# Performance work log

Hardware: AMD Instinct MI355X
Metric: run time of the kernel (lower is better)

## Reference

```python
import jax, jax.numpy as jnp
import numpy as np

NUM_SWEEPS = 200
BETA_MIN = 0.1
BETA_MAX = 5.0


def _anneal(thetas, Jsym, key):
    """Batched simulated annealing over Ising spins in {-1,+1}.

    thetas: [B, N] per-sample biases h; Jsym: [N, N] symmetric couplings.
    Vectorized Metropolis: each sweep, every spin is a flip candidate with
    prob 1/2 (random mask decorrelates simultaneous flips) and is accepted
    with prob min(1, exp(-beta * dE)).
    """
    B, N = thetas.shape
    k0, kloop = jax.random.split(key)
    s0 = jnp.where(jax.random.bernoulli(k0, 0.5, (B, N)), 1.0, -1.0).astype(thetas.dtype)
    betas = jnp.geomspace(BETA_MIN, BETA_MAX, NUM_SWEEPS).astype(thetas.dtype)

    def sweep(carry, beta):
        s, k = carry
        k, k1, k2 = jax.random.split(k, 3)
        # local field: h_i + sum_j Jsym_ij s_j  -> dE for flipping spin i
        local = thetas + s @ Jsym  # [B, N]
        dE = -2.0 * s * local
        accept = jax.random.uniform(k1, (B, N), dtype=s.dtype) < jnp.exp(-beta * dE)
        mask = jax.random.bernoulli(k2, 0.5, (B, N))
        s = jnp.where(accept & mask, -s, s)
        return (s, k), None

    (s, _), _ = jax.lax.scan(sweep, (s0, kloop), betas)
    return s


def setup_inputs() -> dict:
    key = jax.random.key(0)
    k1, k2 = jax.random.split(key)
    B, N = 4096, 256
    thetas = jax.random.normal(k1, (B, N), dtype=jnp.float32)
    gamma = jax.random.normal(k2, (N, N), dtype=jnp.float32) * 0.1
    return {"thetas": thetas, "gamma": gamma}


def reference(thetas, gamma):
    # couplings: strictly upper triangle of gamma (i < j), as in gamma_to_couplings
    J = jnp.triu(gamma, 1)
    Jsym = J + J.T
    s = _anneal(thetas, Jsym, jax.random.key(42))  # [B, N] spins in {-1,+1}
    # Ising energy: E = sum_i h_i s_i + sum_{i<j} J_ij s_i s_j
    energies = jnp.sum(s * thetas, axis=1) + 0.5 * jnp.einsum("bi,ij,bj->b", s, Jsym, s)
    return energies
```

## Files before the change

kernel.cpp:

```cpp
#include <hip/hip_runtime.h>
#include <stdint.h>
#include <math.h>

#define PARTITIONABLE 1

namespace {

constexpr int kB = 4096;
constexpr int kN = 256;
constexpr int kSweeps = 200;
constexpr int kSamp = 16;
constexpr int kBlocks = kB / kSamp;

struct K2 { uint32_t a, b; };

__host__ __device__ constexpr uint32_t crotl(uint32_t x, int d) {
  return (x << d) | (x >> (32 - d));
}

__host__ __device__ constexpr K2 ctf(uint32_t k0, uint32_t k1, uint32_t c0, uint32_t c1) {
  uint32_t ks0 = k0, ks1 = k1, ks2 = k0 ^ k1 ^ 0x1BD11BDAu;
  uint32_t x0 = c0 + ks0, x1 = c1 + ks1;
  const int r0[4] = {13, 15, 26, 6};
  const int r1[4] = {17, 29, 16, 24};
  for (int i = 0; i < 4; ++i) { x0 += x1; x1 = crotl(x1, r0[i]); x1 ^= x0; }
  x0 += ks1; x1 += ks2 + 1u;
  for (int i = 0; i < 4; ++i) { x0 += x1; x1 = crotl(x1, r1[i]); x1 ^= x0; }
  x0 += ks2; x1 += ks0 + 2u;
  for (int i = 0; i < 4; ++i) { x0 += x1; x1 = crotl(x1, r0[i]); x1 ^= x0; }
  x0 += ks0; x1 += ks1 + 3u;
  for (int i = 0; i < 4; ++i) { x0 += x1; x1 = crotl(x1, r1[i]); x1 ^= x0; }
  x0 += ks1; x1 += ks2 + 4u;
  for (int i = 0; i < 4; ++i) { x0 += x1; x1 = crotl(x1, r0[i]); x1 ^= x0; }
  x0 += ks2; x1 += ks0 + 5u;
  return K2{x0, x1};
}

struct KeyTable {
  uint32_t s0k[2];
  uint32_t sk[kSweeps][4];
};

constexpr KeyTable make_keys() {
  KeyTable t{};
  K2 root{0u, 42u};
#if PARTITIONABLE
  K2 k0 = ctf(root.a, root.b, 0u, 0u);
  K2 kl = ctf(root.a, root.b, 0u, 1u);
#else
  K2 p0 = ctf(root.a, root.b, 0u, 2u);
  K2 p1 = ctf(root.a, root.b, 1u, 3u);
  K2 k0{p0.a, p1.a};
  K2 kl{p0.b, p1.b};
#endif
  t.s0k[0] = k0.a; t.s0k[1] = k0.b;
  K2 k = kl;
  for (int s = 0; s < kSweeps; ++s) {
#if PARTITIONABLE
    K2 kn = ctf(k.a, k.b, 0u, 0u);
    K2 k1 = ctf(k.a, k.b, 0u, 1u);
    K2 k2 = ctf(k.a, k.b, 0u, 2u);
#else
    K2 q0 = ctf(k.a, k.b, 0u, 3u);
    K2 q1 = ctf(k.a, k.b, 1u, 4u);
    K2 q2 = ctf(k.a, k.b, 2u, 5u);
    K2 kn{q0.a, q1.a};
    K2 k1{q2.a, q0.b};
    K2 k2{q1.b, q2.b};
#endif
    t.sk[s][0] = k1.a; t.sk[s][1] = k1.b;
    t.sk[s][2] = k2.a; t.sk[s][3] = k2.b;
    k = kn;
  }
  return t;
}

__constant__ KeyTable g_keys = make_keys();

__device__ __forceinline__ uint32_t rng_bits32(uint32_t ka, uint32_t kb, uint32_t m) {
#if PARTITIONABLE
  K2 r = ctf(ka, kb, 0u, m);
  return r.a ^ r.b;
#else
  constexpr uint32_t H = (uint32_t)(kB * kN / 2);
  uint32_t p = (m < H) ? m : (m - H);
  K2 r = ctf(ka, kb, p, p + H);
  return (m < H) ? r.a : r.b;
#endif
}

__device__ __forceinline__ float bits_to_uniform(uint32_t bits) {
  return __uint_as_float((bits >> 9) | 0x3f800000u) - 1.0f;
}

__global__ void prep_kernel(const float* __restrict__ gamma,
                            float* __restrict__ jp,
                            float* __restrict__ betas) {
  int e = blockIdx.x * blockDim.x + threadIdx.x;
  int i = e / kN, j = e % kN;
  float v = 0.0f;
  if (i < j) v = gamma[i * kN + j];
  else if (i > j) v = gamma[j * kN + i];
  int rh = i >> 7, l = (i & 127) >> 1, r = i & 1, c = j >> 3, f = j & 7;
  jp[((rh * 32 + c) * 64 + l) * 16 + r * 8 + f] = v;
  if (e < kSweeps) {
    double l0 = log(0.1), l1 = log(5.0);
    betas[e] = (float)exp(l0 + (l1 - l0) * (double)e / (double)(kSweeps - 1));
  }
}

#define FMIX_LO(a, w, j)                                                      \
  asm("v_fma_mix_f32 %0, %1, %2, %0 op_sel:[0,0,0] op_sel_hi:[1,0,0]"         \
      : "+v"(a) : "v"(w), "v"(j))
#define FMIX_HI(a, w, j)                                                      \
  asm("v_fma_mix_f32 %0, %1, %2, %0 op_sel:[1,0,0] op_sel_hi:[1,0,0]"         \
      : "+v"(a) : "v"(w), "v"(j))

__global__ __launch_bounds__(512) void anneal_kernel(
    const float* __restrict__ thetas, const float* __restrict__ jp,
    const float* __restrict__ betas, float* __restrict__ out) {
  __shared__ __align__(16) unsigned short sh_h[2][kSamp][kN];
  __shared__ __align__(16) uint32_t sh_rand[2][kSamp * kN];
  __shared__ float sh_red[kSamp][4];

  const int tid = threadIdx.x;
  const int lane = tid & 63;
  const int wvid = tid >> 6;
  const bool consumer = (wvid < 4);
  const int b0 = blockIdx.x * kSamp;

  int cur = 0;

  if (consumer) {
    const int cw = wvid;
    const int oct = cw & 1;
    const int rh = cw >> 1;
    const int gbase = oct * 8;
    const int row0 = rh * 128 + 2 * lane;

    float th_[16];
    uint32_t sreg[8];
#pragma unroll
    for (int g = 0; g < 8; ++g) {
      float2 t2 = *(const float2*)&thetas[(b0 + gbase + g) * kN + row0];
      th_[2 * g] = t2.x; th_[2 * g + 1] = t2.y;
    }
#pragma unroll
    for (int g = 0; g < 8; ++g) {
      uint32_t m0 = (uint32_t)((b0 + gbase + g) * kN + row0);
      float u0 = bits_to_uniform(rng_bits32(g_keys.s0k[0], g_keys.s0k[1], m0));
      float u1 = bits_to_uniform(rng_bits32(g_keys.s0k[0], g_keys.s0k[1], m0 + 1));
      uint32_t pk = ((u0 < 0.5f) ? 0x3C00u : 0xBC00u) |
                    (((u1 < 0.5f) ? 0x3C00u : 0xBC00u) << 16);
      sreg[g] = pk;
      *(uint32_t*)&sh_h[0][gbase + g][row0] = pk;
    }
    __syncthreads();

    const float4* __restrict__ jpt =
        (const float4*)jp + (size_t)rh * 8192 + (size_t)lane * 4;

#define LDSPIN(g, c) (*(const uint4*)&sh_h[cur][gbase + (g)][(c) * 8])
#define CONSUME2(W, Q0, Q1, Q2, Q3)                                           \
  _Pragma("unroll")                                                           \
  for (int g = 0; g < 8; ++g) {                                               \
    FMIX_LO(acc[2*g], W[g].x, Q0.x); FMIX_HI(acc[2*g], W[g].x, Q0.y);         \
    FMIX_LO(acc[2*g], W[g].y, Q0.z); FMIX_HI(acc[2*g], W[g].y, Q0.w);         \
    FMIX_LO(acc[2*g], W[g].z, Q1.x); FMIX_HI(acc[2*g], W[g].z, Q1.y);         \
    FMIX_LO(acc[2*g], W[g].w, Q1.z); FMIX_HI(acc[2*g], W[g].w, Q1.w);         \
    FMIX_LO(acc[2*g+1], W[g].x, Q2.x); FMIX_HI(acc[2*g+1], W[g].x, Q2.y);     \
    FMIX_LO(acc[2*g+1], W[g].y, Q2.z); FMIX_HI(acc[2*g+1], W[g].y, Q2.w);     \
    FMIX_LO(acc[2*g+1], W[g].z, Q3.x); FMIX_HI(acc[2*g+1], W[g].z, Q3.y);     \
    FMIX_LO(acc[2*g+1], W[g].w, Q3.z); FMIX_HI(acc[2*g+1], W[g].w, Q3.w);     \
  }
#define MATVEC(acc)                                                           \
  {                                                                           \
    uint4 A[8], Bw[8];                                                        \
    float4 a0, a1, a2, a3, b0_, b1_, b2_, b3_;                                \
    _Pragma("unroll")                                                         \
    for (int g = 0; g < 8; ++g) A[g] = LDSPIN(g, 0);                          \
    a0 = jpt[0]; a1 = jpt[1]; a2 = jpt[2]; a3 = jpt[3];                       \
    _Pragma("unroll 1")                                                       \
    for (int k = 0; k < 15; ++k) {                                            \
      const int c = 2 * k;                                                    \
      _Pragma("unroll")                                                       \
      for (int g = 0; g < 8; ++g) Bw[g] = LDSPIN(g, c + 1);                   \
      b0_ = jpt[(c + 1) * 256 + 0]; b1_ = jpt[(c + 1) * 256 + 1];             \
      b2_ = jpt[(c + 1) * 256 + 2]; b3_ = jpt[(c + 1) * 256 + 3];             \
      CONSUME2(A, a0, a1, a2, a3)                                             \
      _Pragma("unroll")                                                       \
      for (int g = 0; g < 8; ++g) A[g] = LDSPIN(g, c + 2);                    \
      a0 = jpt[(c + 2) * 256 + 0]; a1 = jpt[(c + 2) * 256 + 1];               \
      a2 = jpt[(c + 2) * 256 + 2]; a3 = jpt[(c + 2) * 256 + 3];               \
      CONSUME2(Bw, b0_, b1_, b2_, b3_)                                        \
    }                                                                         \
    _Pragma("unroll")                                                         \
    for (int g = 0; g < 8; ++g) Bw[g] = LDSPIN(g, 31);                        \
    b0_ = jpt[31 * 256 + 0]; b1_ = jpt[31 * 256 + 1];                         \
    b2_ = jpt[31 * 256 + 2]; b3_ = jpt[31 * 256 + 3];                         \
    CONSUME2(A, a0, a1, a2, a3)                                               \
    CONSUME2(Bw, b0_, b1_, b2_, b3_)                                          \
  }

#pragma unroll 1
    for (int t = 0; t < kSweeps; ++t) {
      const float beta = betas[t];
      uint2 wp[8];
      {
        const uint32_t* __restrict__ rb =
            &sh_rand[t & 1][gbase * kN + rh * 128 + 2 * lane];
#pragma unroll
        for (int g = 0; g < 8; ++g)
          wp[g] = *(const uint2*)&rb[g * kN];
      }

      float acc[16];
#pragma unroll
      for (int x = 0; x < 16; ++x) acc[x] = 0.0f;
      MATVEC(acc)

#pragma unroll
      for (int g = 0; g < 8; ++g) {
        uint32_t pk = sreg[g];
        float s0f = __uint_as_float(0x3F800000u | ((pk << 16) & 0x80000000u));
        float s1f = __uint_as_float(0x3F800000u | (pk & 0x80000000u));
        float l0 = th_[2 * g] + acc[2 * g];
        float l1 = th_[2 * g + 1] + acc[2 * g + 1];
        float d0 = -2.0f * s0f * l0;
        float d1 = -2.0f * s1f * l1;
        float p0 = expf(-beta * d0);
        float p1 = expf(-beta * d1);
        float u0 = __uint_as_float((wp[g].x >> 1) | 0x3f800000u) - 1.0f;
        float u1 = __uint_as_float((wp[g].y >> 1) | 0x3f800000u) - 1.0f;
        uint32_t msk = 0u;
        if ((u0 < p0) && ((wp[g].x & 1u) == 0u)) msk |= 0x8000u;
        if ((u1 < p1) && ((wp[g].y & 1u) == 0u)) msk |= 0x80000000u;
        pk ^= msk;
        sreg[g] = pk;
        *(uint32_t*)&sh_h[cur ^ 1][gbase + g][row0] = pk;
      }
      __syncthreads();
      cur ^= 1;
    }

    {
      float acc[16];
#pragma unroll
      for (int x = 0; x < 16; ++x) acc[x] = 0.0f;
      MATVEC(acc)

#pragma unroll
      for (int g = 0; g < 8; ++g) {
        uint32_t pk = sreg[g];
        float s0f = __uint_as_float(0x3F800000u | ((pk << 16) & 0x80000000u));
        float s1f = __uint_as_float(0x3F800000u | (pk & 0x80000000u));
        float x0 = s0f * th_[2 * g] + 0.5f * (s0f * acc[2 * g]);
        float x1 = s1f * th_[2 * g + 1] + 0.5f * (s1f * acc[2 * g + 1]);
#pragma unroll
        for (int off = 16; off > 0; off >>= 1) {
          x0 += __shfl_down(x0, off);
          x1 += __shfl_down(x1, off);
        }
        float v = x0 + x1;
        if (lane == 0)  sh_red[gbase + g][2 * rh + 0] = v;
        if (lane == 32) sh_red[gbase + g][2 * rh + 1] = v;
      }
    }
  } else {
    const int p = (wvid - 4) * 64 + lane;
    {
      const uint32_t k1a = g_keys.sk[0][0], k1b = g_keys.sk[0][1];
      const uint32_t k2a = g_keys.sk[0][2], k2b = g_keys.sk[0][3];
      const uint32_t mb = (uint32_t)(b0 * kN + p * 16);
#pragma unroll 4
      for (int q = 0; q < 16; ++q) {
        uint32_t b1 = rng_bits32(k1a, k1b, mb + q);
        uint32_t b2 = rng_bits32(k2a, k2b, mb + q);
        sh_rand[0][p * 16 + q] = ((b1 >> 9) << 1) | (b2 >> 31);
      }
    }
    __syncthreads();

#pragma unroll 1
    for (int t = 0; t < kSweeps; ++t) {
      if (t + 1 < kSweeps) {
        const uint32_t k1a = g_keys.sk[t + 1][0], k1b = g_keys.sk[t + 1][1];
        const uint32_t k2a = g_keys.sk[t + 1][2], k2b = g_keys.sk[t + 1][3];
        const uint32_t mb = (uint32_t)(b0 * kN + p * 16);
        uint32_t wv[16];
#pragma unroll 4
        for (int q = 0; q < 16; ++q) {
          uint32_t b1 = rng_bits32(k1a, k1b, mb + q);
          uint32_t b2 = rng_bits32(k2a, k2b, mb + q);
          wv[q] = ((b1 >> 9) << 1) | (b2 >> 31);
        }
        uint32_t* dst = &sh_rand[(t + 1) & 1][p * 16];
#pragma unroll
        for (int q = 0; q < 4; ++q) {
          uint4 v; v.x = wv[4*q]; v.y = wv[4*q+1]; v.z = wv[4*q+2]; v.w = wv[4*q+3];
          *(uint4*)(dst + 4 * q) = v;
        }
      }
      __syncthreads();
    }
  }

  __syncthreads();
  if (tid < kSamp) {
    out[b0 + tid] =
        sh_red[tid][0] + sh_red[tid][1] + sh_red[tid][2] + sh_red[tid][3];
  }
}

}

extern "C" void kernel_launch(void* const* d_in, const int* in_sizes, int n_in,
                              void* d_out, int out_size, void* d_ws, size_t ws_size,
                              hipStream_t stream) {
  const float* thetas = (const float*)d_in[0];
  const float* gamma  = (const float*)d_in[1];
  float* jp    = (float*)d_ws;
  float* betas = (float*)((char*)d_ws + kN * kN * sizeof(float));

  hipLaunchKernelGGL(prep_kernel, dim3(kN), dim3(kN), 0, stream, gamma, jp, betas);
  hipLaunchKernelGGL(anneal_kernel, dim3(kBlocks), dim3(512), 0, stream,
                     thetas, jp, betas, (float*)d_out);
}
```

Baseline: 2.218 ms.

## Retile sweep matvec so each wave covers 4 samples across all 256 spins

```diff
diff --git a/kernel.cpp b/kernel.cpp
--- a/kernel.cpp
+++ b/kernel.cpp
@@ -94,18 +94,22 @@
 }
 
 __global__ void prep_kernel(const float* __restrict__ gamma,
-                            float* __restrict__ jp,
+                            float* __restrict__ jpA,
+                            float* __restrict__ jpB,
                             float* __restrict__ betas) {
   int e = blockIdx.x * blockDim.x + threadIdx.x;
   int i = e / kN, j = e % kN;
   float v = 0.0f;
   if (i < j) v = gamma[i * kN + j];
   else if (i > j) v = gamma[j * kN + i];
-  int rh = i >> 7, l = (i & 127) >> 1, r = i & 1, c = j >> 3, f = j & 7;
-  jp[((rh * 32 + c) * 64 + l) * 16 + r * 8 + f] = v;
+  int c = j >> 3, f = j & 7;
+  int l = i >> 2, rp = (i >> 1) & 1, rr = i & 1;
+  jpA[(((c * 64 + l) * 2 + rp) * 2 + rr) * 8 + f] = v;
+  int rh = i >> 7, l2 = (i & 127) >> 1, r = i & 1;
+  jpB[((rh * 32 + c) * 64 + l2) * 16 + r * 8 + f] = v;
   if (e < kSweeps) {
-    double l0 = log(0.1), l1 = log(5.0);
-    betas[e] = (float)exp(l0 + (l1 - l0) * (double)e / (double)(kSweeps - 1));
+    double lo = log(0.1), hi = log(5.0);
+    betas[e] = (float)exp(lo + (hi - lo) * (double)e / (double)(kSweeps - 1));
   }
 }
 
@@ -117,8 +121,9 @@
       : "+v"(a) : "v"(w), "v"(j))
 
 __global__ __launch_bounds__(512) void anneal_kernel(
-    const float* __restrict__ thetas, const float* __restrict__ jp,
-    const float* __restrict__ betas, float* __restrict__ out) {
+    const float* __restrict__ thetas, const float* __restrict__ jpA,
+    const float* __restrict__ jpB, const float* __restrict__ betas,
+    float* __restrict__ out) {
   __shared__ __align__(16) unsigned short sh_h[2][kSamp][kN];
   __shared__ __align__(16) uint32_t sh_rand[2][kSamp * kN];
   __shared__ float sh_red[kSamp][4];
@@ -133,137 +138,191 @@
 
   if (consumer) {
     const int cw = wvid;
-    const int oct = cw & 1;
-    const int rh = cw >> 1;
-    const int gbase = oct * 8;
-    const int row0 = rh * 128 + 2 * lane;
-
-    float th_[16];
-    uint32_t sreg[8];
-#pragma unroll
-    for (int g = 0; g < 8; ++g) {
-      float2 t2 = *(const float2*)&thetas[(b0 + gbase + g) * kN + row0];
-      th_[2 * g] = t2.x; th_[2 * g + 1] = t2.y;
-    }
-#pragma unroll
-    for (int g = 0; g < 8; ++g) {
+    const int gbase = cw * 4;
+    const int row0 = 4 * lane;
+
+    float4 th4[4];
+    uint2 sreg[4];
+#pragma unroll
+    for (int g = 0; g < 4; ++g)
+      th4[g] = *(const float4*)&thetas[(b0 + gbase + g) * kN + row0];
+
+#pragma unroll
+    for (int g = 0; g < 4; ++g) {
       uint32_t m0 = (uint32_t)((b0 + gbase + g) * kN + row0);
-      float u0 = bits_to_uniform(rng_bits32(g_keys.s0k[0], g_keys.s0k[1], m0));
-      float u1 = bits_to_uniform(rng_bits32(g_keys.s0k[0], g_keys.s0k[1], m0 + 1));
-      uint32_t pk = ((u0 < 0.5f) ? 0x3C00u : 0xBC00u) |
-                    (((u1 < 0.5f) ? 0x3C00u : 0xBC00u) << 16);
-      sreg[g] = pk;
-      *(uint32_t*)&sh_h[0][gbase + g][row0] = pk;
+      uint32_t h[4];
+#pragma unroll
+      for (int r = 0; r < 4; ++r) {
+        float u = bits_to_uniform(
+            rng_bits32(g_keys.s0k[0], g_keys.s0k[1], m0 + r));
+        h[r] = (u < 0.5f) ? 0x3C00u : 0xBC00u;
+      }
+      sreg[g].x = h[0] | (h[1] << 16);
+      sreg[g].y = h[2] | (h[3] << 16);
+      *(uint2*)&sh_h[0][gbase + g][row0] = sreg[g];
     }
     __syncthreads();
 
-    const float4* __restrict__ jpt =
-        (const float4*)jp + (size_t)rh * 8192 + (size_t)lane * 4;
-
-#define LDSPIN(g, c) (*(const uint4*)&sh_h[cur][gbase + (g)][(c) * 8])
-#define CONSUME2(W, Q0, Q1, Q2, Q3)                                           \
+    const float4* __restrict__ jpt = (const float4*)jpA + (size_t)lane * 8;
+
+#define LDSPIN4(g, c) (*(const uint4*)&sh_h[cur][gbase + (g)][(c) * 8])
+#define CONSUME4(W, J)                                                        \
   _Pragma("unroll")                                                           \
-  for (int g = 0; g < 8; ++g) {                                               \
-    FMIX_LO(acc[2*g], W[g].x, Q0.x); FMIX_HI(acc[2*g], W[g].x, Q0.y);         \
-    FMIX_LO(acc[2*g], W[g].y, Q0.z); FMIX_HI(acc[2*g], W[g].y, Q0.w);         \
-    FMIX_LO(acc[2*g], W[g].z, Q1.x); FMIX_HI(acc[2*g], W[g].z, Q1.y);         \
-    FMIX_LO(acc[2*g], W[g].w, Q1.z); FMIX_HI(acc[2*g], W[g].w, Q1.w);         \
-    FMIX_LO(acc[2*g+1], W[g].x, Q2.x); FMIX_HI(acc[2*g+1], W[g].x, Q2.y);     \
-    FMIX_LO(acc[2*g+1], W[g].y, Q2.z); FMIX_HI(acc[2*g+1], W[g].y, Q2.w);     \
-    FMIX_LO(acc[2*g+1], W[g].z, Q3.x); FMIX_HI(acc[2*g+1], W[g].z, Q3.y);     \
-    FMIX_LO(acc[2*g+1], W[g].w, Q3.z); FMIX_HI(acc[2*g+1], W[g].w, Q3.w);     \
-  }
-#define MATVEC(acc)                                                           \
+  for (int q = 0; q < 8; ++q) {                                               \
+    const int g_ = q & 3, rp_ = q >> 2;                                       \
+    FMIX_LO(acc[2*q], W[g_].x, J[rp_*4+0].x); FMIX_HI(acc[2*q], W[g_].x, J[rp_*4+0].y); \
+    FMIX_LO(acc[2*q], W[g_].y, J[rp_*4+0].z); FMIX_HI(acc[2*q], W[g_].y, J[rp_*4+0].w); \
+    FMIX_LO(acc[2*q], W[g_].z, J[rp_*4+1].x); FMIX_HI(acc[2*q], W[g_].z, J[rp_*4+1].y); \
+    FMIX_LO(acc[2*q], W[g_].w, J[rp_*4+1].z); FMIX_HI(acc[2*q], W[g_].w, J[rp_*4+1].w); \
+    FMIX_LO(acc[2*q+1], W[g_].x, J[rp_*4+2].x); FMIX_HI(acc[2*q+1], W[g_].x, J[rp_*4+2].y); \
+    FMIX_LO(acc[2*q+1], W[g_].y, J[rp_*4+2].z); FMIX_HI(acc[2*q+1], W[g_].y, J[rp_*4+2].w); \
+    FMIX_LO(acc[2*q+1], W[g_].z, J[rp_*4+3].x); FMIX_HI(acc[2*q+1], W[g_].z, J[rp_*4+3].y); \
+    FMIX_LO(acc[2*q+1], W[g_].w, J[rp_*4+3].z); FMIX_HI(acc[2*q+1], W[g_].w, J[rp_*4+3].w); \
+  }
+#define MATVEC4(acc)                                                          \
   {                                                                           \
-    uint4 A[8], Bw[8];                                                        \
-    float4 a0, a1, a2, a3, b0_, b1_, b2_, b3_;                                \
+    uint4 A[4], Bw[4];                                                        \
+    float4 JA[8], JB[8];                                                      \
     _Pragma("unroll")                                                         \
-    for (int g = 0; g < 8; ++g) A[g] = LDSPIN(g, 0);                          \
-    a0 = jpt[0]; a1 = jpt[1]; a2 = jpt[2]; a3 = jpt[3];                       \
+    for (int g = 0; g < 4; ++g) A[g] = LDSPIN4(g, 0);                         \
+    _Pragma("unroll")                                                         \
+    for (int r = 0; r < 8; ++r) JA[r] = jpt[r];                               \
     _Pragma("unroll 1")                                                       \
     for (int k = 0; k < 15; ++k) {                                            \
       const int c = 2 * k;                                                    \
       _Pragma("unroll")                                                       \
-      for (int g = 0; g < 8; ++g) Bw[g] = LDSPIN(g, c + 1);                   \
-      b0_ = jpt[(c + 1) * 256 + 0]; b1_ = jpt[(c + 1) * 256 + 1];             \
-      b2_ = jpt[(c + 1) * 256 + 2]; b3_ = jpt[(c + 1) * 256 + 3];             \
-      CONSUME2(A, a0, a1, a2, a3)                                             \
+      for (int g = 0; g < 4; ++g) Bw[g] = LDSPIN4(g, c + 1);                  \
       _Pragma("unroll")                                                       \
-      for (int g = 0; g < 8; ++g) A[g] = LDSPIN(g, c + 2);                    \
-      a0 = jpt[(c + 2) * 256 + 0]; a1 = jpt[(c + 2) * 256 + 1];               \
-      a2 = jpt[(c + 2) * 256 + 2]; a3 = jpt[(c + 2) * 256 + 3];               \
-      CONSUME2(Bw, b0_, b1_, b2_, b3_)                                        \
+      for (int r = 0; r < 8; ++r) JB[r] = jpt[(c + 1) * 512 + r];             \
+      CONSUME4(A, JA)                                                         \
+      _Pragma("unroll")                                                       \
+      for (int g = 0; g < 4; ++g) A[g] = LDSPIN4(g, c + 2);                   \
+      _Pragma("unroll")                                                       \
+      for (int r = 0; r < 8; ++r) JA[r] = jpt[(c + 2) * 512 + r];             \
+      CONSUME4(Bw, JB)                                                        \
     }                                                                         \
     _Pragma("unroll")                                                         \
-    for (int g = 0; g < 8; ++g) Bw[g] = LDSPIN(g, 31);                        \
-    b0_ = jpt[31 * 256 + 0]; b1_ = jpt[31 * 256 + 1];                         \
-    b2_ = jpt[31 * 256 + 2]; b3_ = jpt[31 * 256 + 3];                         \
-    CONSUME2(A, a0, a1, a2, a3)                                               \
-    CONSUME2(Bw, b0_, b1_, b2_, b3_)                                          \
+    for (int g = 0; g < 4; ++g) Bw[g] = LDSPIN4(g, 31);                       \
+    _Pragma("unroll")                                                         \
+    for (int r = 0; r < 8; ++r) JB[r] = jpt[31 * 512 + r];                    \
+    CONSUME4(A, JA)                                                           \
+    CONSUME4(Bw, JB)                                                          \
   }
 
 #pragma unroll 1
     for (int t = 0; t < kSweeps; ++t) {
       const float beta = betas[t];
-      uint2 wp[8];
+      uint4 wp[4];
       {
-        const uint32_t* __restrict__ rb =
-            &sh_rand[t & 1][gbase * kN + rh * 128 + 2 * lane];
-#pragma unroll
-        for (int g = 0; g < 8; ++g)
-          wp[g] = *(const uint2*)&rb[g * kN];
+        const uint32_t* __restrict__ rb = &sh_rand[t & 1][row0];
+#pragma unroll
+        for (int g = 0; g < 4; ++g)
+          wp[g] = *(const uint4*)&rb[(gbase + g) * kN];
       }
 
       float acc[16];
 #pragma unroll
       for (int x = 0; x < 16; ++x) acc[x] = 0.0f;
-      MATVEC(acc)
+      MATVEC4(acc)
+
+#pragma unroll
+      for (int g = 0; g < 4; ++g) {
+        uint32_t pk0 = sreg[g].x, pk1 = sreg[g].y;
+        float s0 = __uint_as_float(0x3F800000u | ((pk0 << 16) & 0x80000000u));
+        float s1 = __uint_as_float(0x3F800000u | (pk0 & 0x80000000u));
+        float s2 = __uint_as_float(0x3F800000u | ((pk1 << 16) & 0x80000000u));
+        float s3 = __uint_as_float(0x3F800000u | (pk1 & 0x80000000u));
+        float l0 = th4[g].x + acc[2 * g + 0];
+        float l1 = th4[g].y + acc[2 * g + 1];
+        float l2 = th4[g].z + acc[2 * (g + 4) + 0];
+        float l3 = th4[g].w + acc[2 * (g + 4) + 1];
+        float p0 = expf(-beta * (-2.0f * s0 * l0));
+        float p1 = expf(-beta * (-2.0f * s1 * l1));
+        float p2 = expf(-beta * (-2.0f * s2 * l2));
+        float p3 = expf(-beta * (-2.0f * s3 * l3));
+        float u0 = __uint_as_float((wp[g].x >> 1) | 0x3f800000u) - 1.0f;
+        float u1 = __uint_as_float((wp[g].y >> 1) | 0x3f800000u) - 1.0f;
+        float u2 = __uint_as_float((wp[g].z >> 1) | 0x3f800000u) - 1.0f;
+        float u3 = __uint_as_float((wp[g].w >> 1) | 0x3f800000u) - 1.0f;
+        if ((u0 < p0) && ((wp[g].x & 1u) == 0u)) pk0 ^= 0x8000u;
+        if ((u1 < p1) && ((wp[g].y & 1u) == 0u)) pk0 ^= 0x80000000u;
+        if ((u2 < p2) && ((wp[g].z & 1u) == 0u)) pk1 ^= 0x8000u;
+        if ((u3 < p3) && ((wp[g].w & 1u) == 0u)) pk1 ^= 0x80000000u;
+        sreg[g].x = pk0; sreg[g].y = pk1;
+        *(uint2*)&sh_h[cur ^ 1][gbase + g][row0] = sreg[g];
+      }
+      __syncthreads();
+      cur ^= 1;
+    }
+
+    {
+      const int oct = cw & 1, rh = cw >> 1;
+      const int gb8 = oct * 8;
+      const int row0f = rh * 128 + 2 * lane;
+      const float4* __restrict__ jptf =
+          (const float4*)jpB + (size_t)rh * 8192 + (size_t)lane * 4;
+
+      float accf[16];
+#pragma unroll
+      for (int x = 0; x < 16; ++x) accf[x] = 0.0f;
+
+#define LDSPIN8(g, c) (*(const uint4*)&sh_h[cur][gb8 + (g)][(c) * 8])
+#define CONSUME2F(W, Q0, Q1, Q2, Q3)                                          \
+  _Pragma("unroll")                                                           \
+  for (int g = 0; g < 8; ++g) {                                               \
+    FMIX_LO(accf[2*g], W[g].x, Q0.x); FMIX_HI(accf[2*g], W[g].x, Q0.y);       \
+    FMIX_LO(accf[2*g], W[g].y, Q0.z); FMIX_HI(accf[2*g], W[g].y, Q0.w);       \
+    FMIX_LO(accf[2*g], W[g].z, Q1.x); FMIX_HI(accf[2*g], W[g].z, Q1.y);       \
+    FMIX_LO(accf[2*g], W[g].w, Q1.z); FMIX_HI(accf[2*g], W[g].w, Q1.w);       \
+    FMIX_LO(accf[2*g+1], W[g].x, Q2.x); FMIX_HI(accf[2*g+1], W[g].x, Q2.y);   \
+    FMIX_LO(accf[2*g+1], W[g].y, Q2.z); FMIX_HI(accf[2*g+1], W[g].y, Q2.w);   \
+    FMIX_LO(accf[2*g+1], W[g].z, Q3.x); FMIX_HI(accf[2*g+1], W[g].z, Q3.y);   \
+    FMIX_LO(accf[2*g+1], W[g].w, Q3.z); FMIX_HI(accf[2*g+1], W[g].w, Q3.w);   \
+  }
+      {
+        uint4 A[8], Bw[8];
+        float4 a0, a1, a2, a3, b0_, b1_, b2_, b3_;
+#pragma unroll
+        for (int g = 0; g < 8; ++g) A[g] = LDSPIN8(g, 0);
+        a0 = jptf[0]; a1 = jptf[1]; a2 = jptf[2]; a3 = jptf[3];
+#pragma unroll 1
+        for (int k = 0; k < 15; ++k) {
+          const int c = 2 * k;
+#pragma unroll
+          for (int g = 0; g < 8; ++g) Bw[g] = LDSPIN8(g, c + 1);
+          b0_ = jptf[(c + 1) * 256 + 0]; b1_ = jptf[(c + 1) * 256 + 1];
+          b2_ = jptf[(c + 1) * 256 + 2]; b3_ = jptf[(c + 1) * 256 + 3];
+          CONSUME2F(A, a0, a1, a2, a3)
+#pragma unroll
+          for (int g = 0; g < 8; ++g) A[g] = LDSPIN8(g, c + 2);
+          a0 = jptf[(c + 2) * 256 + 0]; a1 = jptf[(c + 2) * 256 + 1];
+          a2 = jptf[(c + 2) * 256 + 2]; a3 = jptf[(c + 2) * 256 + 3];
+          CONSUME2F(Bw, b0_, b1_, b2_, b3_)
+        }
+#pragma unroll
+        for (int g = 0; g < 8; ++g) Bw[g] = LDSPIN8(g, 31);
+        b0_ = jptf[31 * 256 + 0]; b1_ = jptf[31 * 256 + 1];
+        b2_ = jptf[31 * 256 + 2]; b3_ = jptf[31 * 256 + 3];
+        CONSUME2F(A, a0, a1, a2, a3)
+        CONSUME2F(Bw, b0_, b1_, b2_, b3_)
+      }
 
 #pragma unroll
       for (int g = 0; g < 8; ++g) {
-        uint32_t pk = sreg[g];
+        uint32_t pk = *(const uint32_t*)&sh_h[cur][gb8 + g][row0f];
+        float2 t2 = *(const float2*)&thetas[(b0 + gb8 + g) * kN + row0f];
         float s0f = __uint_as_float(0x3F800000u | ((pk << 16) & 0x80000000u));
         float s1f = __uint_as_float(0x3F800000u | (pk & 0x80000000u));
-        float l0 = th_[2 * g] + acc[2 * g];
-        float l1 = th_[2 * g + 1] + acc[2 * g + 1];
-        float d0 = -2.0f * s0f * l0;
-        float d1 = -2.0f * s1f * l1;
-        float p0 = expf(-beta * d0);
-        float p1 = expf(-beta * d1);
-        float u0 = __uint_as_float((wp[g].x >> 1) | 0x3f800000u) - 1.0f;
-        float u1 = __uint_as_float((wp[g].y >> 1) | 0x3f800000u) - 1.0f;
-        uint32_t msk = 0u;
-        if ((u0 < p0) && ((wp[g].x & 1u) == 0u)) msk |= 0x8000u;
-        if ((u1 < p1) && ((wp[g].y & 1u) == 0u)) msk |= 0x80000000u;
-        pk ^= msk;
-        sreg[g] = pk;
-        *(uint32_t*)&sh_h[cur ^ 1][gbase + g][row0] = pk;
-      }
-      __syncthreads();
-      cur ^= 1;
-    }
-
-    {
-      float acc[16];
-#pragma unroll
-      for (int x = 0; x < 16; ++x) acc[x] = 0.0f;
-      MATVEC(acc)
-
-#pragma unroll
-      for (int g = 0; g < 8; ++g) {
-        uint32_t pk = sreg[g];
-        float s0f = __uint_as_float(0x3F800000u | ((pk << 16) & 0x80000000u));
-        float s1f = __uint_as_float(0x3F800000u | (pk & 0x80000000u));
-        float x0 = s0f * th_[2 * g] + 0.5f * (s0f * acc[2 * g]);
-        float x1 = s1f * th_[2 * g + 1] + 0.5f * (s1f * acc[2 * g + 1]);
+        float x0 = s0f * t2.x + 0.5f * (s0f * accf[2 * g]);
+        float x1 = s1f * t2.y + 0.5f * (s1f * accf[2 * g + 1]);
 #pragma unroll
         for (int off = 16; off > 0; off >>= 1) {
           x0 += __shfl_down(x0, off);
           x1 += __shfl_down(x1, off);
         }
         float v = x0 + x1;
-        if (lane == 0)  sh_red[gbase + g][2 * rh + 0] = v;
-        if (lane == 32) sh_red[gbase + g][2 * rh + 1] = v;
+        if (lane == 0)  sh_red[gb8 + g][2 * rh + 0] = v;
+        if (lane == 32) sh_red[gb8 + g][2 * rh + 1] = v;
       }
     }
   } else {
@@ -319,10 +378,13 @@
                               hipStream_t stream) {
   const float* thetas = (const float*)d_in[0];
   const float* gamma  = (const float*)d_in[1];
-  float* jp    = (float*)d_ws;
-  float* betas = (float*)((char*)d_ws + kN * kN * sizeof(float));
-
-  hipLaunchKernelGGL(prep_kernel, dim3(kN), dim3(kN), 0, stream, gamma, jp, betas);
+  char* ws = (char*)d_ws;
+  float* jpA   = (float*)ws;
+  float* jpB   = (float*)(ws + (size_t)kN * kN * 4);
+  float* betas = (float*)(ws + (size_t)kN * kN * 8);
+
+  hipLaunchKernelGGL(prep_kernel, dim3(kN), dim3(kN), 0, stream,
+                     gamma, jpA, jpB, betas);
   hipLaunchKernelGGL(anneal_kernel, dim3(kBlocks), dim3(512), 0, stream,
-                     thetas, jp, betas, (float*)d_out);
-}
+                     thetas, jpA, jpB, betas, (float*)d_out);
+}
```

After: 5.705 ms. +157.2%, slower.
